# Kernel tuning notes

Hardware: AMD Instinct MI355X
Metric: run time of the kernel (lower is better)

## Reference

```python
import jax, jax.numpy as jnp
import numpy as np

N = 100000    # nodes ('paper')
E = 600000    # edges per relation
R = 3         # relations (etypes)
IN = 256      # in_feats
HF = 256      # h_feats
H = 4         # n_heads
D = HF // H   # per-head dim
C = 153       # num_classes
NEG_SLOPE = 0.2


def setup_inputs() -> dict:
    key = jax.random.key(0)
    ks = jax.random.split(key, 14)
    s = 0.05
    x = jax.random.normal(ks[0], (N, IN), jnp.float32)
    src = jax.random.randint(ks[1], (R, E), 0, N, jnp.int32)
    dst = jax.random.randint(ks[2], (R, E), 0, N, jnp.int32)
    # layer 1 params (per relation): fc weight, attn_l, attn_r, bias
    W1 = jax.random.normal(ks[3], (R, IN, HF), jnp.float32) * s
    al1 = jax.random.normal(ks[4], (R, H, D), jnp.float32) * s
    ar1 = jax.random.normal(ks[5], (R, H, D), jnp.float32) * s
    b1 = jax.random.normal(ks[6], (R, HF), jnp.float32) * s
    # layer 2 params
    W2 = jax.random.normal(ks[7], (R, HF, HF), jnp.float32) * s
    al2 = jax.random.normal(ks[8], (R, H, D), jnp.float32) * s
    ar2 = jax.random.normal(ks[9], (R, H, D), jnp.float32) * s
    b2 = jax.random.normal(ks[10], (R, HF), jnp.float32) * s
    # output linear
    Wout = jax.random.normal(ks[11], (HF, C), jnp.float32) * s
    bout = jax.random.normal(ks[12], (C,), jnp.float32) * s
    return {"x": x, "src": src, "dst": dst,
            "W1": W1, "al1": al1, "ar1": ar1, "b1": b1,
            "W2": W2, "al2": al2, "ar2": ar2, "b2": b2,
            "Wout": Wout, "bout": bout}


def _hetero_gat_layer(h, src, dst, W, al, ar, b):
    """HeteroGraphConv over R relations of GATConv, aggregate='sum'.
    h: [N, F_in] -> returns [N, H, D]."""
    acc = jnp.zeros((N, H, D), h.dtype)
    for r in range(R):  # small fixed relation set
        sr, dr = src[r], dst[r]
        feat = (h @ W[r]).reshape(N, H, D)           # projected [N,H,D]
        el = jnp.sum(feat * al[r], axis=-1)          # [N,H]
        er = jnp.sum(feat * ar[r], axis=-1)          # [N,H]
        e = jax.nn.leaky_relu(el[sr] + er[dr], NEG_SLOPE)  # [E,H]
        # edge softmax per destination node, per head
        m = jax.ops.segment_max(e, dr, num_segments=N)     # [N,H]
        a = jnp.exp(e - m[dr])                             # [E,H]
        z = jax.ops.segment_sum(a, dr, num_segments=N)     # [N,H]
        alpha = a / z[dr]                                  # [E,H]
        msg = feat[sr] * alpha[:, :, None]                 # [E,H,D]
        out = jax.ops.segment_sum(msg, dr, num_segments=N) # [N,H,D]
        acc = acc + out + b[r].reshape(1, H, D)
    return acc


def reference(x, src, dst, W1, al1, ar1, b1, W2, al2, ar2, b2, Wout, bout):
    h = _hetero_gat_layer(x, src, dst, W1, al1, ar1, b1).reshape(N, HF)
    h = jax.nn.relu(h)  # apply_each(h, F.relu); dropout is identity in eval
    h = _hetero_gat_layer(h, src, dst, W2, al2, ar2, b2).reshape(N, HF)
    return h @ Wout + bout  # self.linear(h['paper'])
```

## Files before the change

kernel.cpp:

```cpp
#include <hip/hip_runtime.h>
#include <hip/hip_bf16.h>

#define NN 100000
#define EE 600000
#define RR 3
#define INF 256
#define HFF 256
#define NH 4
#define DD 64
#define CC 153
#define NB 98

typedef __attribute__((ext_vector_type(8))) _Float16 f16x8;
typedef __attribute__((ext_vector_type(4))) float f32x4;

#define GLDS(g, l) __builtin_amdgcn_global_load_lds((const __attribute__((address_space(1))) void*)(g), \
                                                    (__attribute__((address_space(3))) void*)(l), 16, 0, 0)

static __device__ __forceinline__ unsigned short f2h(float x) {
    _Float16 h = (_Float16)x;
    return __builtin_bit_cast(unsigned short, h);
}
static __device__ __forceinline__ float h2f(unsigned short u) {
    return (float)__builtin_bit_cast(_Float16, u);
}

template<int GM>
__global__ __launch_bounds__(256) void mfma_gemm(const unsigned short* __restrict__ A,
                                                 const unsigned short* __restrict__ Bt,
                                                 const float* __restrict__ bias,
                                                 float* __restrict__ C32,
                                                 unsigned short* __restrict__ C16,
                                                 const float* __restrict__ al,
                                                 const float* __restrict__ ar,
                                                 float* __restrict__ el,
                                                 float* __restrict__ er,
                                                 int M) {
    __shared__ __align__(1024) char lds[32768];
    const int tid = threadIdx.x;
    const int lane = tid & 63;
    const int w = tid >> 6;
    const int wr = w >> 1, wc = w & 1;
    const int bm = blockIdx.x * 128;
    const int bn = blockIdx.y * 128;

    f32x4 acc[4][4] = {};

    const int lrow8 = lane >> 3;
    const int cbs = ((lane & 7) << 4) ^ ((lrow8 & 7) << 4);
    const int cbase = w * 8;
    const bool isA = (w < 2);

    const char* gA = (const char*)A;
    const char* gB = (const char*)Bt;

    for (int step = 0; step < 4; ++step) {
        const int k0b = step * 128;
#pragma unroll
        for (int i = 0; i < 8; ++i) {
            int c = cbase + i;
            char* lptr = &lds[c * 1024];
            if (isA) {
                int R = c * 8 + lrow8;
                int grow = bm + R; if (grow >= M) grow = M - 1;
                GLDS(gA + (size_t)grow * 512 + k0b + cbs, lptr);
            } else {
                int nIdx = (c - 16) * 8 + lrow8;
                GLDS(gB + (size_t)(bn + nIdx) * 512 + k0b + cbs, lptr);
            }
        }
        __syncthreads();
#pragma unroll
        for (int kk = 0; kk < 2; ++kk) {
            f16x8 af[4], bfr[4];
            const int o = kk * 64 + ((lane >> 4) << 4);
#pragma unroll
            for (int m = 0; m < 4; ++m) {
                int R = wr * 64 + m * 16 + (lane & 15);
                af[m] = *reinterpret_cast<const f16x8*>(&lds[R * 128 + (o ^ ((R & 7) << 4))]);
            }
#pragma unroll
            for (int n = 0; n < 4; ++n) {
                int Rn = wc * 64 + n * 16 + (lane & 15);
                bfr[n] = *reinterpret_cast<const f16x8*>(&lds[16384 + Rn * 128 + (o ^ ((Rn & 7) << 4))]);
            }
#pragma unroll
            for (int m = 0; m < 4; ++m)
#pragma unroll
                for (int n = 0; n < 4; ++n)
                    acc[m][n] = __builtin_amdgcn_mfma_f32_16x16x32_f16(af[m], bfr[n], acc[m][n], 0, 0, 0);
        }
        __syncthreads();
    }

    const int rb = bm + wr * 64 + ((lane >> 4) << 2);

    if (GM == 0) {
        const int cb2 = bn + wc * 64 + (lane & 15);
#pragma unroll
        for (int m = 0; m < 4; ++m)
#pragma unroll
            for (int n = 0; n < 4; ++n) {
                int col = cb2 + n * 16;
                if (col < CC) {
                    float bb = bias[col];
#pragma unroll
                    for (int j = 0; j < 4; ++j) {
                        int row = rb + m * 16 + j;
                        if (row < M) C32[(size_t)row * CC + col] = acc[m][n][j] + bb;
                    }
                }
            }
    } else {
        const int h = (bn >> 6) + wc;
        float alv[4], arv[4];
#pragma unroll
        for (int n = 0; n < 4; ++n) {
            alv[n] = al[h * 64 + n * 16 + (lane & 15)];
            arv[n] = ar[h * 64 + n * 16 + (lane & 15)];
        }
#pragma unroll
        for (int m = 0; m < 4; ++m)
#pragma unroll
            for (int j = 0; j < 4; ++j) {
                float pl = acc[m][0][j] * alv[0] + acc[m][1][j] * alv[1]
                         + acc[m][2][j] * alv[2] + acc[m][3][j] * alv[3];
                float pr = acc[m][0][j] * arv[0] + acc[m][1][j] * arv[1]
                         + acc[m][2][j] * arv[2] + acc[m][3][j] * arv[3];
#pragma unroll
                for (int o2 = 1; o2 < 16; o2 <<= 1) {
                    pl += __shfl_xor(pl, o2);
                    pr += __shfl_xor(pr, o2);
                }
                int row = rb + m * 16 + j;
                if ((lane & 15) == 0 && row < M) {
                    el[row * 4 + h] = pl;
                    er[row * 4 + h] = pr;
                }
            }
        const int cb2 = bn + wc * 64 + (lane & 15);
#pragma unroll
        for (int m = 0; m < 4; ++m)
#pragma unroll
            for (int n = 0; n < 4; ++n) {
                int col = cb2 + n * 16;
#pragma unroll
                for (int j = 0; j < 4; ++j) {
                    int row = rb + m * 16 + j;
                    if (row < M) C16[(size_t)row * 256 + col] = f2h(acc[m][n][j]);
                }
            }
    }
}

__global__ __launch_bounds__(256) void f2h4(const float* __restrict__ in,
                                            unsigned short* __restrict__ out, int n4) {
    int i = blockIdx.x * 256 + threadIdx.x;
    if (i >= n4) return;
    float4 v = reinterpret_cast<const float4*>(in)[i];
    ushort4 o;
    o.x = f2h(v.x); o.y = f2h(v.y); o.z = f2h(v.z); o.w = f2h(v.w);
    reinterpret_cast<ushort4*>(out)[i] = o;
}

__global__ __launch_bounds__(256) void wt_kernel(const float* __restrict__ W,
                                                 unsigned short* __restrict__ Wt) {
    int idx = blockIdx.x * 256 + threadIdx.x;
    if (idx >= RR * 65536) return;
    int r = idx >> 16, rem = idx & 65535;
    int n = rem >> 8, k = rem & 255;
    Wt[idx] = f2h(W[(r << 16) + (k << 8) + n]);
}

__global__ __launch_bounds__(256) void wout_kernel(const float* __restrict__ Wout,
                                                   unsigned short* __restrict__ Wt) {
    int idx = blockIdx.x * 256 + threadIdx.x;
    if (idx >= 65536) return;
    int n = idx >> 8, k = idx & 255;
    Wt[idx] = (n < CC) ? f2h(Wout[k * CC + n]) : (unsigned short)0;
}

__global__ __launch_bounds__(256) void hist_kernel(const int* __restrict__ dst,
                                                   int* __restrict__ deg) {
    int i = blockIdx.x * 256 + threadIdx.x;
    if (i >= RR * EE) return;
    int r = i / EE;
    atomicAdd(&deg[r * NN + dst[i]], 1);
}

__global__ __launch_bounds__(256) void scan_block(const int* __restrict__ deg,
                                                  int* __restrict__ rowptr,
                                                  int* __restrict__ bsum) {
    __shared__ int sh[256];
    int r = blockIdx.y, b = blockIdx.x, t = threadIdx.x;
    int base = b * 1024;
    int v[4];
#pragma unroll
    for (int j = 0; j < 4; ++j) {
        int idx = base + t * 4 + j;
        v[j] = (idx < NN) ? deg[r * NN + idx] : 0;
    }
    int tsum = v[0] + v[1] + v[2] + v[3];
    sh[t] = tsum;
    __syncthreads();
    for (int off = 1; off < 256; off <<= 1) {
        int x = (t >= off) ? sh[t - off] : 0;
        __syncthreads();
        sh[t] += x;
        __syncthreads();
    }
    int run = sh[t] - tsum;
#pragma unroll
    for (int j = 0; j < 4; ++j) {
        int idx = base + t * 4 + j;
        if (idx < NN) rowptr[r * (NN + 1) + idx] = run;
        run += v[j];
    }
    if (t == 255) bsum[r * NB + b] = run;
}

__global__ void scan_bsum(int* __restrict__ bsum, int* __restrict__ rowptr) {
    int r = threadIdx.x;
    if (r >= RR) return;
    int run = 0;
    for (int b = 0; b < NB; ++b) {
        int x = bsum[r * NB + b];
        bsum[r * NB + b] = run;
        run += x;
    }
    rowptr[r * (NN + 1) + NN] = run;
}

__global__ __launch_bounds__(256) void add_off(int* __restrict__ rowptr,
                                               const int* __restrict__ bsum) {
    int r = blockIdx.y, b = blockIdx.x, t = threadIdx.x;
    int o = bsum[r * NB + b];
#pragma unroll
    for (int j = 0; j < 4; ++j) {
        int idx = b * 1024 + t * 4 + j;
        if (idx < NN) rowptr[r * (NN + 1) + idx] += o;
    }
}

__global__ __launch_bounds__(256) void fill_kernel(const int* __restrict__ src,
                                                   const int* __restrict__ dst,
                                                   const int* __restrict__ rowptr,
                                                   int* __restrict__ cursor,
                                                   int* __restrict__ csrc) {
    int i = blockIdx.x * 256 + threadIdx.x;
    if (i >= RR * EE) return;
    int r = i / EE;
    int d = dst[i], s = src[i];
    int pos = rowptr[r * (NN + 1) + d] + atomicAdd(&cursor[r * NN + d], 1);
    csrc[(size_t)r * EE + pos] = s;
}

template<int RELU>
__global__ __launch_bounds__(256) void agg3_kernel(const int* __restrict__ csrc,
                                                   const int* __restrict__ rowptr,
                                                   const float* __restrict__ el,
                                                   const float* __restrict__ er,
                                                   const unsigned short* __restrict__ feat,
                                                   const float* __restrict__ brel,
                                                   unsigned short* __restrict__ hout) {
    int wid = (blockIdx.x * 256 + threadIdx.x) >> 6;
    int lane = threadIdx.x & 63;
    if (wid >= NN) return;
    int d = wid;
    int h = lane >> 4;
    int f0 = lane * 4;

    float4 bA = *reinterpret_cast<const float4*>(brel + f0);
    float4 bB = *reinterpret_cast<const float4*>(brel + 256 + f0);
    float4 bC = *reinterpret_cast<const float4*>(brel + 512 + f0);
    float4 cur = make_float4(bA.x + bB.x + bC.x, bA.y + bB.y + bC.y,
                             bA.z + bB.z + bC.z, bA.w + bB.w + bC.w);

#pragma unroll
    for (int r = 0; r < RR; ++r) {
        int p0 = rowptr[r * (NN + 1) + d], p1 = rowptr[r * (NN + 1) + d + 1];
        if (p0 == p1) continue;
        float erd = er[(size_t)r * NN * 4 + d * 4 + h];
        const float* elr = el + (size_t)r * NN * 4;
        const unsigned short* fr = feat + (size_t)r * NN * 256;
        const int* cs = csrc + (size_t)r * EE;

        float4 accA = make_float4(0.f, 0.f, 0.f, 0.f);
        float4 accB = make_float4(0.f, 0.f, 0.f, 0.f);
        float zs = 0.f;
        int last = p1 - 1;
        for (int p = p0; p < p1; p += 4) {
            int q1 = p + 1 <= last ? p + 1 : last;
            int q2 = p + 2 <= last ? p + 2 : last;
            int q3 = p + 3 <= last ? p + 3 : last;
            int s0 = cs[p], s1 = cs[q1], s2 = cs[q2], s3 = cs[q3];
            ushort4 fA = *reinterpret_cast<const ushort4*>(fr + (size_t)s0 * 256 + f0);
            ushort4 fB = *reinterpret_cast<const ushort4*>(fr + (size_t)s1 * 256 + f0);
            ushort4 fC = *reinterpret_cast<const ushort4*>(fr + (size_t)s2 * 256 + f0);
            ushort4 fD = *reinterpret_cast<const ushort4*>(fr + (size_t)s3 * 256 + f0);
            float v0 = elr[s0 * 4 + h] + erd;
            float v1 = elr[s1 * 4 + h] + erd;
            float v2 = elr[s2 * 4 + h] + erd;
            float v3 = elr[s3 * 4 + h] + erd;
            v0 = v0 > 0.f ? v0 : 0.2f * v0;
            v1 = v1 > 0.f ? v1 : 0.2f * v1;
            v2 = v2 > 0.f ? v2 : 0.2f * v2;
            v3 = v3 > 0.f ? v3 : 0.2f * v3;
            float w0 = __expf(v0);
            float w1 = (p + 1 <= last) ? __expf(v1) : 0.f;
            float w2 = (p + 2 <= last) ? __expf(v2) : 0.f;
            float w3 = (p + 3 <= last) ? __expf(v3) : 0.f;
            zs += (w0 + w1) + (w2 + w3);
            accA.x += w0 * h2f(fA.x); accA.y += w0 * h2f(fA.y);
            accA.z += w0 * h2f(fA.z); accA.w += w0 * h2f(fA.w);
            accB.x += w1 * h2f(fB.x); accB.y += w1 * h2f(fB.y);
            accB.z += w1 * h2f(fB.z); accB.w += w1 * h2f(fB.w);
            accA.x += w2 * h2f(fC.x); accA.y += w2 * h2f(fC.y);
            accA.z += w2 * h2f(fC.z); accA.w += w2 * h2f(fC.w);
            accB.x += w3 * h2f(fD.x); accB.y += w3 * h2f(fD.y);
            accB.z += w3 * h2f(fD.z); accB.w += w3 * h2f(fD.w);
        }
        float inv = 1.f / zs;
        cur.x += (accA.x + accB.x) * inv;
        cur.y += (accA.y + accB.y) * inv;
        cur.z += (accA.z + accB.z) * inv;
        cur.w += (accA.w + accB.w) * inv;
    }
    if (RELU) {
        cur.x = fmaxf(cur.x, 0.f); cur.y = fmaxf(cur.y, 0.f);
        cur.z = fmaxf(cur.z, 0.f); cur.w = fmaxf(cur.w, 0.f);
    }
    ushort4 o;
    o.x = f2h(cur.x); o.y = f2h(cur.y); o.z = f2h(cur.z); o.w = f2h(cur.w);
    *reinterpret_cast<ushort4*>(hout + (size_t)d * 256 + f0) = o;
}

extern "C" void kernel_launch(void* const* d_in, const int* in_sizes, int n_in,
                              void* d_out, int out_size, void* d_ws, size_t ws_size,
                              hipStream_t stream) {
    const float* x    = (const float*)d_in[0];
    const int*   src  = (const int*)d_in[1];
    const int*   dst  = (const int*)d_in[2];
    const float* W1   = (const float*)d_in[3];
    const float* al1  = (const float*)d_in[4];
    const float* ar1  = (const float*)d_in[5];
    const float* b1   = (const float*)d_in[6];
    const float* W2   = (const float*)d_in[7];
    const float* al2  = (const float*)d_in[8];
    const float* ar2  = (const float*)d_in[9];
    const float* b2   = (const float*)d_in[10];
    const float* Wout = (const float*)d_in[11];
    const float* bout = (const float*)d_in[12];
    float* out = (float*)d_out;

    char* base = (char*)d_ws;
    size_t off = 0;
    auto alloc = [&](size_t bytes) -> char* {
        char* p = base + off;
        off = (off + bytes + 255) & ~(size_t)255;
        return p;
    };
    size_t NF = (size_t)NN * HFF;
    unsigned short* feath = (unsigned short*)alloc(RR * NF * 2);
    float* el   = (float*)alloc((size_t)RR * NN * NH * 4);
    float* er   = (float*)alloc((size_t)RR * NN * NH * 4);
    int* deg    = (int*)alloc((size_t)RR * NN * 4 * 2);
    int* cursor = deg + (size_t)RR * NN;
    int* rowptr = (int*)alloc((size_t)RR * (NN + 1) * 4);
    int* bsum   = (int*)alloc((size_t)RR * NB * 4);
    int* csrc   = (int*)alloc((size_t)RR * EE * 4);
    unsigned short* xh    = (unsigned short*)alloc(NF * 2);
    unsigned short* wth   = (unsigned short*)alloc((size_t)2 * RR * 65536 * 2);
    unsigned short* wouth = (unsigned short*)alloc((size_t)65536 * 2);

    int n4Blocks = (int)((NF / 4 + 255) / 256);
    int reBlocks = (RR * EE + 255) / 256;
    int aggBlocks = (NN * 64 + 255) / 256;
    dim3 ggrid((NN + 127) / 128, 2);

    hipMemsetAsync(deg, 0, (size_t)RR * NN * sizeof(int) * 2, stream);
    hist_kernel<<<reBlocks, 256, 0, stream>>>(dst, deg);
    scan_block<<<dim3(NB, RR), 256, 0, stream>>>(deg, rowptr, bsum);
    scan_bsum<<<1, 64, 0, stream>>>(bsum, rowptr);
    add_off<<<dim3(NB, RR), 256, 0, stream>>>(rowptr, bsum);
    fill_kernel<<<reBlocks, 256, 0, stream>>>(src, dst, rowptr, cursor, csrc);

    f2h4<<<n4Blocks, 256, 0, stream>>>(x, xh, (int)(NF / 4));
    wt_kernel<<<(RR * 65536) / 256, 256, 0, stream>>>(W1, wth);
    wt_kernel<<<(RR * 65536) / 256, 256, 0, stream>>>(W2, wth + (size_t)RR * 65536);
    wout_kernel<<<65536 / 256, 256, 0, stream>>>(Wout, wouth);

    for (int layer = 0; layer < 2; ++layer) {
        const float* al = layer ? al2 : al1;
        const float* ar = layer ? ar2 : ar1;
        const float* b  = layer ? b2 : b1;
        const unsigned short* wl = wth + (size_t)layer * RR * 65536;

        for (int r = 0; r < RR; ++r)
            mfma_gemm<1><<<ggrid, 256, 0, stream>>>(xh, wl + (size_t)r * 65536, nullptr,
                                                    nullptr, feath + (size_t)r * NF,
                                                    al + r * NH * DD, ar + r * NH * DD,
                                                    el + (size_t)r * NN * NH,
                                                    er + (size_t)r * NN * NH, NN);
        if (layer == 0)
            agg3_kernel<1><<<aggBlocks, 256, 0, stream>>>(csrc, rowptr, el, er, feath, b, xh);
        else
            agg3_kernel<0><<<aggBlocks, 256, 0, stream>>>(csrc, rowptr, el, er, feath, b, xh);
    }

    mfma_gemm<0><<<ggrid, 256, 0, stream>>>(xh, wouth, bout, out, nullptr,
                                            nullptr, nullptr, nullptr, nullptr, NN);
}
```

Measured before the change: 875.0 us.

## Batch relation GEMMs, stage fp16 output via LDS, and use packed half accumulation

After: 813.9 us. 1.08x faster.

```diff
diff --git a/kernel.cpp b/kernel.cpp
--- a/kernel.cpp
+++ b/kernel.cpp
@@ -12,6 +12,7 @@
 #define NB 98
 
 typedef __attribute__((ext_vector_type(8))) _Float16 f16x8;
+typedef __attribute__((ext_vector_type(2))) _Float16 h2f16;
 typedef __attribute__((ext_vector_type(4))) float f32x4;
 
 #define GLDS(g, l) __builtin_amdgcn_global_load_lds((const __attribute__((address_space(1))) void*)(g), \
@@ -112,12 +113,15 @@
                 }
             }
     } else {
-        const int h = (bn >> 6) + wc;
+        const int c0 = bn + wc * 64;
+        const int rh = c0 >> 6;
+        const int rw = rh >> 2;
+        const int h  = rh & 3;
         float alv[4], arv[4];
 #pragma unroll
         for (int n = 0; n < 4; ++n) {
-            alv[n] = al[h * 64 + n * 16 + (lane & 15)];
-            arv[n] = ar[h * 64 + n * 16 + (lane & 15)];
+            alv[n] = al[rh * 64 + n * 16 + (lane & 15)];
+            arv[n] = ar[rh * 64 + n * 16 + (lane & 15)];
         }
 #pragma unroll
         for (int m = 0; m < 4; ++m)
@@ -134,22 +138,40 @@
                 }
                 int row = rb + m * 16 + j;
                 if ((lane & 15) == 0 && row < M) {
-                    el[row * 4 + h] = pl;
-                    er[row * 4 + h] = pr;
+                    el[(size_t)rw * NN * 4 + row * 4 + h] = pl;
+                    er[(size_t)rw * NN * 4 + row * 4 + h] = pr;
                 }
             }
-        const int cb2 = bn + wc * 64 + (lane & 15);
+        __syncthreads();
+        unsigned short* l16 = (unsigned short*)lds;
 #pragma unroll
         for (int m = 0; m < 4; ++m)
 #pragma unroll
-            for (int n = 0; n < 4; ++n) {
-                int col = cb2 + n * 16;
+            for (int n = 0; n < 4; ++n)
 #pragma unroll
                 for (int j = 0; j < 4; ++j) {
-                    int row = rb + m * 16 + j;
-                    if (row < M) C16[(size_t)row * 256 + col] = f2h(acc[m][n][j]);
+                    int row = wr * 64 + m * 16 + ((lane >> 4) << 2) + j;
+                    int colb = (wc * 64 + n * 16 + (lane & 15)) * 2;
+                    int addr = row * 256 + (colb ^ (((row >> 2) & 7) << 5));
+                    l16[addr >> 1] = f2h(acc[m][n][j]);
                 }
-            }
+        __syncthreads();
+        const int rblk = bn >> 8;
+        const int bnc  = bn & 255;
+        const size_t NFE = (size_t)NN * 256;
+#pragma unroll
+        for (int i = 0; i < 8; ++i) {
+            int seg = w * 8 + i;
+            int row = seg * 4 + (lane >> 4);
+            int colb = (lane & 15) * 16;
+            int addr = row * 256 + (colb ^ (((row >> 2) & 7) << 5));
+            uint4 v = *reinterpret_cast<const uint4*>(&lds[addr]);
+            int grow = bm + row;
+            if (grow < M) {
+                unsigned short* gp = C16 + (size_t)rblk * NFE + (size_t)grow * 256 + bnc + (lane & 15) * 8;
+                *reinterpret_cast<uint4*>(gp) = v;
+            }
+        }
     }
 }
 
@@ -285,8 +307,8 @@
         const unsigned short* fr = feat + (size_t)r * NN * 256;
         const int* cs = csrc + (size_t)r * EE;
 
-        float4 accA = make_float4(0.f, 0.f, 0.f, 0.f);
-        float4 accB = make_float4(0.f, 0.f, 0.f, 0.f);
+        h2f16 aA01 = (h2f16)0, aA23 = (h2f16)0;
+        h2f16 aB01 = (h2f16)0, aB23 = (h2f16)0;
         float zs = 0.f;
         int last = p1 - 1;
         for (int p = p0; p < p1; p += 4) {
@@ -294,10 +316,10 @@
             int q2 = p + 2 <= last ? p + 2 : last;
             int q3 = p + 3 <= last ? p + 3 : last;
             int s0 = cs[p], s1 = cs[q1], s2 = cs[q2], s3 = cs[q3];
-            ushort4 fA = *reinterpret_cast<const ushort4*>(fr + (size_t)s0 * 256 + f0);
-            ushort4 fB = *reinterpret_cast<const ushort4*>(fr + (size_t)s1 * 256 + f0);
-            ushort4 fC = *reinterpret_cast<const ushort4*>(fr + (size_t)s2 * 256 + f0);
-            ushort4 fD = *reinterpret_cast<const ushort4*>(fr + (size_t)s3 * 256 + f0);
+            uint2 fA = *reinterpret_cast<const uint2*>(fr + (size_t)s0 * 256 + f0);
+            uint2 fB = *reinterpret_cast<const uint2*>(fr + (size_t)s1 * 256 + f0);
+            uint2 fC = *reinterpret_cast<const uint2*>(fr + (size_t)s2 * 256 + f0);
+            uint2 fD = *reinterpret_cast<const uint2*>(fr + (size_t)s3 * 256 + f0);
             float v0 = elr[s0 * 4 + h] + erd;
             float v1 = elr[s1 * 4 + h] + erd;
             float v2 = elr[s2 * 4 + h] + erd;
@@ -311,20 +333,24 @@
             float w2 = (p + 2 <= last) ? __expf(v2) : 0.f;
             float w3 = (p + 3 <= last) ? __expf(v3) : 0.f;
             zs += (w0 + w1) + (w2 + w3);
-            accA.x += w0 * h2f(fA.x); accA.y += w0 * h2f(fA.y);
-            accA.z += w0 * h2f(fA.z); accA.w += w0 * h2f(fA.w);
-            accB.x += w1 * h2f(fB.x); accB.y += w1 * h2f(fB.y);
-            accB.z += w1 * h2f(fB.z); accB.w += w1 * h2f(fB.w);
-            accA.x += w2 * h2f(fC.x); accA.y += w2 * h2f(fC.y);
-            accA.z += w2 * h2f(fC.z); accA.w += w2 * h2f(fC.w);
-            accB.x += w3 * h2f(fD.x); accB.y += w3 * h2f(fD.y);
-            accB.z += w3 * h2f(fD.z); accB.w += w3 * h2f(fD.w);
+            _Float16 h0 = (_Float16)w0, h1 = (_Float16)w1;
+            _Float16 h2 = (_Float16)w2, h3 = (_Float16)w3;
+            h2f16 wp0 = (h2f16){h0, h0}, wp1 = (h2f16){h1, h1};
+            h2f16 wp2 = (h2f16){h2, h2}, wp3 = (h2f16){h3, h3};
+            aA01 += wp0 * __builtin_bit_cast(h2f16, fA.x);
+            aA23 += wp0 * __builtin_bit_cast(h2f16, fA.y);
+            aB01 += wp1 * __builtin_bit_cast(h2f16, fB.x);
+            aB23 += wp1 * __builtin_bit_cast(h2f16, fB.y);
+            aA01 += wp2 * __builtin_bit_cast(h2f16, fC.x);
+            aA23 += wp2 * __builtin_bit_cast(h2f16, fC.y);
+            aB01 += wp3 * __builtin_bit_cast(h2f16, fD.x);
+            aB23 += wp3 * __builtin_bit_cast(h2f16, fD.y);
         }
         float inv = 1.f / zs;
-        cur.x += (accA.x + accB.x) * inv;
-        cur.y += (accA.y + accB.y) * inv;
-        cur.z += (accA.z + accB.z) * inv;
-        cur.w += (accA.w + accB.w) * inv;
+        cur.x += ((float)aA01[0] + (float)aB01[0]) * inv;
+        cur.y += ((float)aA01[1] + (float)aB01[1]) * inv;
+        cur.z += ((float)aA23[0] + (float)aB23[0]) * inv;
+        cur.w += ((float)aA23[1] + (float)aB23[1]) * inv;
     }
     if (RELU) {
         cur.x = fmaxf(cur.x, 0.f); cur.y = fmaxf(cur.y, 0.f);
@@ -376,7 +402,8 @@
     int n4Blocks = (int)((NF / 4 + 255) / 256);
     int reBlocks = (RR * EE + 255) / 256;
     int aggBlocks = (NN * 64 + 255) / 256;
-    dim3 ggrid((NN + 127) / 128, 2);
+    dim3 pgrid((NN + 127) / 128, 6);
+    dim3 ogrid((NN + 127) / 128, 2);
 
     hipMemsetAsync(deg, 0, (size_t)RR * NN * sizeof(int) * 2, stream);
     hist_kernel<<<reBlocks, 256, 0, stream>>>(dst, deg);
@@ -396,18 +423,14 @@
         const float* b  = layer ? b2 : b1;
         const unsigned short* wl = wth + (size_t)layer * RR * 65536;
 
-        for (int r = 0; r < RR; ++r)
-            mfma_gemm<1><<<ggrid, 256, 0, stream>>>(xh, wl + (size_t)r * 65536, nullptr,
-                                                    nullptr, feath + (size_t)r * NF,
-                                                    al + r * NH * DD, ar + r * NH * DD,
-                                                    el + (size_t)r * NN * NH,
-                                                    er + (size_t)r * NN * NH, NN);
+        mfma_gemm<1><<<pgrid, 256, 0, stream>>>(xh, wl, nullptr,
+                                                nullptr, feath, al, ar, el, er, NN);
         if (layer == 0)
             agg3_kernel<1><<<aggBlocks, 256, 0, stream>>>(csrc, rowptr, el, er, feath, b, xh);
         else
             agg3_kernel<0><<<aggBlocks, 256, 0, stream>>>(csrc, rowptr, el, er, feath, b, xh);
     }
 
-    mfma_gemm<0><<<ggrid, 256, 0, stream>>>(xh, wouth, bout, out, nullptr,
+    mfma_gemm<0><<<ogrid, 256, 0, stream>>>(xh, wouth, bout, out, nullptr,
                                             nullptr, nullptr, nullptr, nullptr, NN);
 }
```
